# Performance work log

Hardware: AMD Instinct MI355X
Metric: run time of the kernel (lower is better)

The kernel has to match this reference:

```python
import jax, jax.numpy as jnp
import numpy as np

N_NODES = 50000
N_EDGES = 800000


def _gcn_norm(edge_index, n_nodes):
    # add self-loops, compute symmetric normalization D^-1/2 (A+I) D^-1/2
    loops = jnp.arange(n_nodes, dtype=edge_index.dtype)
    row = jnp.concatenate([edge_index[0], loops])
    col = jnp.concatenate([edge_index[1], loops])
    deg = jax.ops.segment_sum(jnp.ones_like(row, dtype=jnp.float32), row,
                              num_segments=n_nodes)
    dinv = jnp.where(deg > 0, jax.lax.rsqrt(deg), 0.0)
    norm = dinv[row] * dinv[col]  # [E+N]
    return row, col, norm


def _gcn_conv(x, W, b, row, col, norm, n_nodes):
    h = x @ W                                  # [N, out] transform first (cheaper gather)
    msg = norm[:, None] * h[col]               # [E+N, out]
    agg = jax.ops.segment_sum(msg, row, num_segments=n_nodes)
    return agg + b


def setup_inputs() -> dict:
    key = jax.random.key(0)
    ks = jax.random.split(key, 8)
    F_in, H, F_out = 64, 128, 64
    return {
        "features": jax.random.normal(ks[0], (N_NODES, F_in), jnp.float32),
        "W1": jax.random.normal(ks[1], (F_in, H), jnp.float32) / np.sqrt(F_in),
        "b1": jnp.zeros((H,), jnp.float32),
        "W2": jax.random.normal(ks[2], (H, H), jnp.float32) / np.sqrt(H),
        "b2": jnp.zeros((H,), jnp.float32),
        "W3": jax.random.normal(ks[3], (H, F_out), jnp.float32) / np.sqrt(H),
        "b3": jnp.zeros((F_out,), jnp.float32),
        "edge_index": jax.random.randint(ks[4], (2, N_EDGES), 0, N_NODES, jnp.int32),
    }


def reference(features, W1, b1, W2, b2, W3, b3, edge_index):
    n = features.shape[0]
    row, col, norm = _gcn_norm(edge_index, n)
    x = jax.nn.relu(_gcn_conv(features, W1, b1, row, col, norm, n))
    x = jax.nn.relu(_gcn_conv(x, W2, b2, row, col, norm, n))
    x = _gcn_conv(x, W3, b3, row, col, norm, n)
    return x
```

## Files before the change

### kernel.cpp

```cpp
#include <hip/hip_runtime.h>

#define N_NODES 50000
#define N_EDGES 800000

#define SCAN_CHUNK 256
#define SCAN_BLOCKS ((N_NODES + SCAN_CHUNK - 1) / SCAN_CHUNK)

static inline size_t alignUp(size_t x, size_t a) { return (x + a - 1) & ~(a - 1); }

typedef _Float16 h2 __attribute__((ext_vector_type(2)));
typedef _Float16 h4 __attribute__((ext_vector_type(4)));


__global__ void k_zero_i32(int* __restrict__ p, int n) {
    int i = blockIdx.x * 256 + threadIdx.x;
    if (i < n) p[i] = 0;
}

__global__ void k_count4(const int* __restrict__ row, int* __restrict__ count,
                         int* __restrict__ rank, int* __restrict__ pad) {
    int i = blockIdx.x * 256 + threadIdx.x;
    if (i < 64) pad[i] = 0;
    if (i < N_EDGES / 4) {
        int4 r = reinterpret_cast<const int4*>(row)[i];
        int k0 = atomicAdd(&count[r.x], 1);
        int k1 = atomicAdd(&count[r.y], 1);
        int k2 = atomicAdd(&count[r.z], 1);
        int k3 = atomicAdd(&count[r.w], 1);
        reinterpret_cast<int4*>(rank)[i] = make_int4(k0, k1, k2, k3);
    }
}

__global__ void k_blocksum(const int* __restrict__ count, int* __restrict__ bsum) {
    __shared__ int s[256];
    int t = threadIdx.x;
    int i = blockIdx.x * 256 + t;
    int v = (i < N_NODES) ? count[i] : 0;
    s[t] = v;
    __syncthreads();
    for (int off = 128; off > 0; off >>= 1) {
        if (t < off) s[t] += s[t + off];
        __syncthreads();
    }
    if (t == 0) bsum[blockIdx.x] = s[0];
}

__global__ void k_scan_bsum(int* __restrict__ bsum) {
    __shared__ int s[256];
    int t = threadIdx.x;
    int v = (t < SCAN_BLOCKS) ? bsum[t] : 0;
    s[t] = v;
    __syncthreads();
    for (int off = 1; off < 256; off <<= 1) {
        int add = (t >= off) ? s[t - off] : 0;
        __syncthreads();
        s[t] += add;
        __syncthreads();
    }
    if (t < SCAN_BLOCKS) bsum[t] = s[t] - v;
}

__global__ void k_scan_final(const int* __restrict__ count, const int* __restrict__ bsum,
                             int* __restrict__ offsets, float* __restrict__ dinv) {
    __shared__ int s[256];
    int t = threadIdx.x;
    int i = blockIdx.x * 256 + t;
    int v = (i < N_NODES) ? count[i] : 0;
    s[t] = v;
    __syncthreads();
    for (int off = 1; off < 256; off <<= 1) {
        int add = (t >= off) ? s[t - off] : 0;
        __syncthreads();
        s[t] += add;
        __syncthreads();
    }
    if (i < N_NODES) {
        offsets[i] = s[t] - v + bsum[blockIdx.x];
        dinv[i]    = rsqrtf((float)(v + 1));
    }
}

__global__ void k_scatter(const int* __restrict__ row, const int* __restrict__ col,
                          const int* __restrict__ offsets, const int* __restrict__ rank,
                          int* __restrict__ csr_col,
                          const float* __restrict__ feat, const float* __restrict__ dinv,
                          _Float16* __restrict__ featS) {
    int e = blockIdx.x * 256 + threadIdx.x;
    if (e < N_EDGES) {
        int node = e >> 4;
        float d = dinv[node];
        float4 v = reinterpret_cast<const float4*>(feat)[e];
        h4 hv = {(_Float16)(v.x * d), (_Float16)(v.y * d),
                 (_Float16)(v.z * d), (_Float16)(v.w * d)};
        reinterpret_cast<h4*>(featS)[e] = hv;
        int r = row[e];
        csr_col[offsets[r] + rank[e]] = col[e];
    }
}


template <bool BIAS>
__global__ __launch_bounds__(256) void k_agg128(const _Float16* __restrict__ hs, float* __restrict__ out,
        const int* __restrict__ csr_col, const int* __restrict__ offsets,
        const int* __restrict__ count, const float* __restrict__ dinv,
        const float* __restrict__ bias) {
    int lane = threadIdx.x & 63;
    int node = blockIdx.x * 4 + (threadIdx.x >> 6);
    const char* base = (const char*)hs;
    uint32_t lo = (uint32_t)lane << 2;

    float ax[8], ay[8];
#pragma unroll
    for (int u = 0; u < 8; u++) { ax[u] = 0.f; ay[u] = 0.f; }

    int n = count[node];
    const int* cp = csr_col + offsets[node];

    int e = 0;
    for (; e + 8 <= n; e += 8) {
        int c[8];
#pragma unroll
        for (int u = 0; u < 8; u++) c[u] = cp[e + u];
#pragma unroll
        for (int u = 0; u < 8; u++) {
            h2 v = *reinterpret_cast<const h2*>(base + (((uint32_t)c[u] << 8) + lo));
            ax[u] += (float)v.x; ay[u] += (float)v.y;
        }
    }
    if (e < n) {
        int c[8];
#pragma unroll
        for (int u = 0; u < 8; u++) c[u] = cp[e + u];
#pragma unroll
        for (int u = 0; u < 8; u++) {
            h2 v = *reinterpret_cast<const h2*>(base + (((uint32_t)c[u] << 8) + lo));
            if (e + u < n) { ax[u] += (float)v.x; ay[u] += (float)v.y; }
        }
    }

    float sx = 0.f, sy = 0.f;
#pragma unroll
    for (int u = 0; u < 8; u++) { sx += ax[u]; sy += ay[u]; }
    h2 self = *reinterpret_cast<const h2*>(base + (((uint32_t)node << 8) + lo));
    float d = dinv[node];
    float ox = (sx + (float)self.x) * d, oy = (sy + (float)self.y) * d;
    if (BIAS) { ox += bias[2 * lane]; oy += bias[2 * lane + 1]; }
    reinterpret_cast<float2*>(out)[(size_t)node * 64 + lane] = make_float2(ox, oy);
}

template <bool BIAS>
__global__ __launch_bounds__(256) void k_agg64(const _Float16* __restrict__ hs, float* __restrict__ out,
        const int* __restrict__ csr_col, const int* __restrict__ offsets,
        const int* __restrict__ count, const float* __restrict__ dinv,
        const float* __restrict__ bias) {
    int lane = threadIdx.x & 63;
    int node = blockIdx.x * 4 + (threadIdx.x >> 6);
    int q = lane >> 4;
    int f4 = lane & 15;
    const char* base = (const char*)hs;
    uint32_t fo = (uint32_t)f4 << 3;

    int n = __builtin_amdgcn_readfirstlane(count[node]);
    int start = __builtin_amdgcn_readfirstlane(offsets[node]);
    const int* cp = csr_col + start;

    float4 a0 = make_float4(0.f, 0.f, 0.f, 0.f);
    float4 a1 = make_float4(0.f, 0.f, 0.f, 0.f);

    int e = 0;
    for (; e + 32 <= n; e += 32) {
        int c[8];
#pragma unroll
        for (int u = 0; u < 8; u++) c[u] = cp[e + 4 * u + q];
        h4 v[8];
#pragma unroll
        for (int u = 0; u < 8; u++)
            v[u] = *reinterpret_cast<const h4*>(base + (((uint32_t)c[u] << 7) + fo));
#pragma unroll
        for (int u = 0; u < 8; u += 2) {
            a0.x += (float)v[u].x; a0.y += (float)v[u].y;
            a0.z += (float)v[u].z; a0.w += (float)v[u].w;
            a1.x += (float)v[u+1].x; a1.y += (float)v[u+1].y;
            a1.z += (float)v[u+1].z; a1.w += (float)v[u+1].w;
        }
    }
    if (e < n) {
        int c[8];
#pragma unroll
        for (int u = 0; u < 8; u++) c[u] = cp[e + 4 * u + q];
        h4 v[8];
#pragma unroll
        for (int u = 0; u < 8; u++)
            v[u] = *reinterpret_cast<const h4*>(base + (((uint32_t)c[u] << 7) + fo));
#pragma unroll
        for (int u = 0; u < 8; u++) {
            if (e + 4 * u + q < n) {
                a0.x += (float)v[u].x; a0.y += (float)v[u].y;
                a0.z += (float)v[u].z; a0.w += (float)v[u].w;
            }
        }
    }

    float sx = a0.x + a1.x, sy = a0.y + a1.y, sz = a0.z + a1.z, sw = a0.w + a1.w;
    sx += __shfl_xor(sx, 16); sy += __shfl_xor(sy, 16);
    sz += __shfl_xor(sz, 16); sw += __shfl_xor(sw, 16);
    sx += __shfl_xor(sx, 32); sy += __shfl_xor(sy, 32);
    sz += __shfl_xor(sz, 32); sw += __shfl_xor(sw, 32);
    if (q == 0) {
        h4 self = *reinterpret_cast<const h4*>(base + (((uint32_t)node << 7) + fo));
        float d = dinv[node];
        float ox = (sx + (float)self.x) * d, oy = (sy + (float)self.y) * d;
        float oz = (sz + (float)self.z) * d, ow = (sw + (float)self.w) * d;
        if (BIAS) {
            float4 bv = *reinterpret_cast<const float4*>(&bias[f4 * 4]);
            ox += bv.x; oy += bv.y; oz += bv.z; ow += bv.w;
        }
        *reinterpret_cast<float4*>((char*)out + ((uint32_t)node << 8) + (fo << 1)) =
            make_float4(ox, oy, oz, ow);
    }
}


template <int K, int NOUT, int BM, bool RELU, bool BIAS, bool SCALE, bool HOUT>
__global__ __launch_bounds__(256, 4) void k_gemm(const float* __restrict__ x,
        const float* __restrict__ W, const float* __restrict__ bias,
        const float* __restrict__ dinv, void* __restrict__ out, int nrows) {
    constexpr int BK = 32, BN = 64;
    constexpr int NCB = NOUT / BN;
    constexpr int RPT = BM / 16;
    __shared__ float xt[BK * BM];
    __shared__ float wt[BK * BN];

    int tid = threadIdx.x;
    int rg = tid & 15;
    int cg = tid >> 4;
    int row0 = (blockIdx.x / NCB) * BM;
    int col0 = (blockIdx.x % NCB) * BN;

    float acc[RPT][4] = {};

#pragma unroll 1
    for (int kk = 0; kk < K; kk += BK) {
        __syncthreads();
#pragma unroll
        for (int t = 0; t < BM / 32; ++t) {
            int idx = tid + t * 256;
            int r = idx >> 3;
            int kc = (idx & 7) * 4;
            float4 v = make_float4(0.f, 0.f, 0.f, 0.f);
            int gr = row0 + r;
            if (gr < nrows) v = *reinterpret_cast<const float4*>(&x[(size_t)gr * K + kk + kc]);
            int rc = r ^ kc;
            xt[(kc + 0) * BM + rc] = v.x;
            xt[(kc + 1) * BM + rc] = v.y;
            xt[(kc + 2) * BM + rc] = v.z;
            xt[(kc + 3) * BM + rc] = v.w;
        }
#pragma unroll
        for (int t = 0; t < 2; ++t) {
            int idx = tid + t * 256;
            int k = idx >> 4;
            int c = (idx & 15) * 4;
            *reinterpret_cast<float4*>(&wt[k * BN + c]) =
                *reinterpret_cast<const float4*>(&W[(size_t)(kk + k) * NOUT + col0 + c]);
        }
        __syncthreads();

#pragma unroll
        for (int k = 0; k < BK; ++k) {
            int s = k & 28;
            float4 wv = *reinterpret_cast<const float4*>(&wt[k * BN + cg * 4]);
            float wr[4] = {wv.x, wv.y, wv.z, wv.w};
            float xr[RPT];
            float4 x0 = *reinterpret_cast<const float4*>(&xt[k * BM + ((rg * 4) ^ s)]);
            xr[0] = x0.x; xr[1] = x0.y; xr[2] = x0.z; xr[3] = x0.w;
            if constexpr (RPT == 8) {
                float4 x1 = *reinterpret_cast<const float4*>(&xt[k * BM + (((rg * 4) ^ s) + 64)]);
                xr[4] = x1.x; xr[5] = x1.y; xr[6] = x1.z; xr[7] = x1.w;
            }
#pragma unroll
            for (int a = 0; a < RPT; a++)
#pragma unroll
                for (int b = 0; b < 4; b++) acc[a][b] += xr[a] * wr[b];
        }
    }

    float bv[4];
    if (BIAS) {
#pragma unroll
        for (int b = 0; b < 4; b++) bv[b] = bias[col0 + cg * 4 + b];
    }
#pragma unroll
    for (int a = 0; a < RPT; a++) {
        int r = rg * 4 + (a & 3) + ((a >= 4) ? 64 : 0);
        int gr = row0 + r;
        if (gr >= nrows) continue;
        float d = SCALE ? dinv[gr] : 1.f;
        float o[4];
#pragma unroll
        for (int b = 0; b < 4; b++) {
            float v = acc[a][b];
            if (BIAS) v += bv[b];
            if (RELU) v = fmaxf(v, 0.f);
            o[b] = v * d;
        }
        if constexpr (HOUT) {
            h4 ho = {(_Float16)o[0], (_Float16)o[1], (_Float16)o[2], (_Float16)o[3]};
            *reinterpret_cast<h4*>((_Float16*)out + (size_t)gr * NOUT + col0 + cg * 4) = ho;
        } else {
            *reinterpret_cast<float4*>((float*)out + (size_t)gr * NOUT + col0 + cg * 4) =
                make_float4(o[0], o[1], o[2], o[3]);
        }
    }
}


extern "C" void kernel_launch(void* const* d_in, const int* in_sizes, int n_in,
                              void* d_out, int out_size, void* d_ws, size_t ws_size,
                              hipStream_t stream) {
    const float* feat = (const float*)d_in[0];
    const float* W1 = (const float*)d_in[1];
    const float* b1 = (const float*)d_in[2];
    const float* W2 = (const float*)d_in[3];
    const float* b2 = (const float*)d_in[4];
    const float* W3 = (const float*)d_in[5];
    const float* b3 = (const float*)d_in[6];
    const int* ei = (const int*)d_in[7];
    const int* row = ei;
    const int* col = ei + N_EDGES;
    float* out = (float*)d_out;

    char* ws = (char*)d_ws;
    size_t off = 0;
    auto alloc = [&](size_t bytes) {
        void* p = ws + off;
        off = alignUp(off + bytes, 256);
        return p;
    };
    float* B0      = (float*)alloc((size_t)N_NODES * 128 * 4);
    float* B1      = (float*)alloc((size_t)N_NODES * 128 * 4);
    float* dinv    = (float*)alloc((size_t)N_NODES * 4);
    int*   count   = (int*)alloc((size_t)N_NODES * 4);
    int*   offsets = (int*)alloc((size_t)N_NODES * 4);
    int*   bsum    = (int*)alloc(1024);
    int*   csr_col = (int*)alloc((size_t)(N_EDGES + 64) * 4);
    int* rank = (int*)B0;
    _Float16* featS = (_Float16*)B1;
    _Float16* B1h = (_Float16*)B1;
    _Float16* B0h = (_Float16*)B0;

    const int eb = (N_EDGES + 255) / 256;
    const int cb4 = (N_EDGES / 4 + 255) / 256;
    const int rb128 = (N_NODES + 127) / 128;
    const int rb64  = (N_NODES + 63) / 64;
    const int agg_grid = N_NODES / 4;

    k_zero_i32<<<(N_NODES + 255) / 256, 256, 0, stream>>>(count, N_NODES);
    k_count4<<<cb4, 256, 0, stream>>>(row, count, rank, csr_col + N_EDGES);
    k_blocksum<<<SCAN_BLOCKS, 256, 0, stream>>>(count, bsum);
    k_scan_bsum<<<1, 256, 0, stream>>>(bsum);
    k_scan_final<<<SCAN_BLOCKS, 256, 0, stream>>>(count, bsum, offsets, dinv);
    k_scatter<<<eb, 256, 0, stream>>>(row, col, offsets, rank, csr_col, feat, dinv, featS);

    k_agg64<false><<<agg_grid, 256, 0, stream>>>(featS, B0, csr_col, offsets, count, dinv, nullptr);
    k_gemm<64, 128, 128, true, true, true, true><<<rb128 * 2, 256, 0, stream>>>(B0, W1, b1, dinv, B1h, N_NODES);

    k_agg128<false><<<agg_grid, 256, 0, stream>>>(B1h, B0, csr_col, offsets, count, dinv, nullptr);
    k_gemm<128, 128, 128, true, true, false, false><<<rb128 * 2, 256, 0, stream>>>(B0, W2, b2, dinv, B1, N_NODES);

    k_gemm<128, 64, 64, false, false, true, true><<<rb64, 256, 0, stream>>>(B1, W3, nullptr, dinv, B0h, N_NODES);
    k_agg64<true><<<agg_grid, 256, 0, stream>>>(B0h, out, csr_col, offsets, count, dinv, b3);
}
```

Before: 221.3 us.

## Replace FP32 SIMT GEMMs with FP16 MFMA GEMMs and store intermediates as FP16

The shared-memory FP32 tiled GEMM is replaced with a kernel that calls the 16x16x32 f16 MFMA instruction directly, reading A rows and pre-transposed FP16 weights straight from global memory. A new small kernel converts and transposes W1..W3 to FP16 on each call. The aggregation kernels gain an FP16 output mode, so every intermediate activation buffer is half precision, which halves the memory traffic between the aggregate and GEMM stages. In exchange, aggregated sums and the layer-2 output are rounded to FP16, which costs accuracy, and the GEMM gives up shared-memory reuse of the weight tile.

```diff
diff --git a/kernel.cpp b/kernel.cpp
--- a/kernel.cpp
+++ b/kernel.cpp
@@ -10,6 +10,8 @@
 
 typedef _Float16 h2 __attribute__((ext_vector_type(2)));
 typedef _Float16 h4 __attribute__((ext_vector_type(4)));
+typedef _Float16 h8 __attribute__((ext_vector_type(8)));
+typedef float    f4 __attribute__((ext_vector_type(4)));
 
 
 __global__ void k_zero_i32(int* __restrict__ p, int n) {
@@ -99,8 +101,25 @@
 }
 
 
-template <bool BIAS>
-__global__ __launch_bounds__(256) void k_agg128(const _Float16* __restrict__ hs, float* __restrict__ out,
+__global__ void k_prepw(const float* __restrict__ W1, const float* __restrict__ W2,
+                        const float* __restrict__ W3, _Float16* __restrict__ W1T,
+                        _Float16* __restrict__ W2T, _Float16* __restrict__ W3T) {
+    int i = blockIdx.x * 256 + threadIdx.x;
+    if (i < 8192) {
+        int n = i >> 6, k = i & 63;
+        W1T[i] = (_Float16)W1[k * 128 + n];
+    } else if (i < 24576) {
+        int j = i - 8192; int n = j >> 7, k = j & 127;
+        W2T[j] = (_Float16)W2[k * 128 + n];
+    } else {
+        int j = i - 24576; int n = j >> 7, k = j & 127;
+        W3T[j] = (_Float16)W3[k * 64 + n];
+    }
+}
+
+
+template <bool BIAS, bool HOUT>
+__global__ __launch_bounds__(256) void k_agg128(const _Float16* __restrict__ hs, void* __restrict__ out,
         const int* __restrict__ csr_col, const int* __restrict__ offsets,
         const int* __restrict__ count, const float* __restrict__ dinv,
         const float* __restrict__ bias) {
@@ -145,11 +164,16 @@
     float d = dinv[node];
     float ox = (sx + (float)self.x) * d, oy = (sy + (float)self.y) * d;
     if (BIAS) { ox += bias[2 * lane]; oy += bias[2 * lane + 1]; }
-    reinterpret_cast<float2*>(out)[(size_t)node * 64 + lane] = make_float2(ox, oy);
-}
-
-template <bool BIAS>
-__global__ __launch_bounds__(256) void k_agg64(const _Float16* __restrict__ hs, float* __restrict__ out,
+    if constexpr (HOUT) {
+        h2 hv = {(_Float16)ox, (_Float16)oy};
+        reinterpret_cast<h2*>(out)[(size_t)node * 64 + lane] = hv;
+    } else {
+        reinterpret_cast<float2*>(out)[(size_t)node * 64 + lane] = make_float2(ox, oy);
+    }
+}
+
+template <bool BIAS, bool HOUT>
+__global__ __launch_bounds__(256) void k_agg64(const _Float16* __restrict__ hs, void* __restrict__ out,
         const int* __restrict__ csr_col, const int* __restrict__ offsets,
         const int* __restrict__ count, const float* __restrict__ dinv,
         const float* __restrict__ bias) {
@@ -215,101 +239,64 @@
             float4 bv = *reinterpret_cast<const float4*>(&bias[f4 * 4]);
             ox += bv.x; oy += bv.y; oz += bv.z; ow += bv.w;
         }
-        *reinterpret_cast<float4*>((char*)out + ((uint32_t)node << 8) + (fo << 1)) =
-            make_float4(ox, oy, oz, ow);
-    }
-}
-
-
-template <int K, int NOUT, int BM, bool RELU, bool BIAS, bool SCALE, bool HOUT>
-__global__ __launch_bounds__(256, 4) void k_gemm(const float* __restrict__ x,
-        const float* __restrict__ W, const float* __restrict__ bias,
+        if constexpr (HOUT) {
+            h4 hv = {(_Float16)ox, (_Float16)oy, (_Float16)oz, (_Float16)ow};
+            *reinterpret_cast<h4*>((char*)out + (((uint32_t)node << 7) + fo)) = hv;
+        } else {
+            *reinterpret_cast<float4*>((char*)out + ((uint32_t)node << 8) + (fo << 1)) =
+                make_float4(ox, oy, oz, ow);
+        }
+    }
+}
+
+
+template <int K, int NOUT, bool RELU, bool BIAS, bool SCALE, bool HOUT>
+__global__ __launch_bounds__(256) void k_gemm_mfma(const _Float16* __restrict__ x,
+        const _Float16* __restrict__ WT, const float* __restrict__ bias,
         const float* __restrict__ dinv, void* __restrict__ out, int nrows) {
-    constexpr int BK = 32, BN = 64;
-    constexpr int NCB = NOUT / BN;
-    constexpr int RPT = BM / 16;
-    __shared__ float xt[BK * BM];
-    __shared__ float wt[BK * BN];
-
-    int tid = threadIdx.x;
-    int rg = tid & 15;
-    int cg = tid >> 4;
-    int row0 = (blockIdx.x / NCB) * BM;
-    int col0 = (blockIdx.x % NCB) * BN;
-
-    float acc[RPT][4] = {};
-
-#pragma unroll 1
-    for (int kk = 0; kk < K; kk += BK) {
-        __syncthreads();
-#pragma unroll
-        for (int t = 0; t < BM / 32; ++t) {
-            int idx = tid + t * 256;
-            int r = idx >> 3;
-            int kc = (idx & 7) * 4;
-            float4 v = make_float4(0.f, 0.f, 0.f, 0.f);
-            int gr = row0 + r;
-            if (gr < nrows) v = *reinterpret_cast<const float4*>(&x[(size_t)gr * K + kk + kc]);
-            int rc = r ^ kc;
-            xt[(kc + 0) * BM + rc] = v.x;
-            xt[(kc + 1) * BM + rc] = v.y;
-            xt[(kc + 2) * BM + rc] = v.z;
-            xt[(kc + 3) * BM + rc] = v.w;
-        }
-#pragma unroll
-        for (int t = 0; t < 2; ++t) {
-            int idx = tid + t * 256;
-            int k = idx >> 4;
-            int c = (idx & 15) * 4;
-            *reinterpret_cast<float4*>(&wt[k * BN + c]) =
-                *reinterpret_cast<const float4*>(&W[(size_t)(kk + k) * NOUT + col0 + c]);
-        }
-        __syncthreads();
-
-#pragma unroll
-        for (int k = 0; k < BK; ++k) {
-            int s = k & 28;
-            float4 wv = *reinterpret_cast<const float4*>(&wt[k * BN + cg * 4]);
-            float wr[4] = {wv.x, wv.y, wv.z, wv.w};
-            float xr[RPT];
-            float4 x0 = *reinterpret_cast<const float4*>(&xt[k * BM + ((rg * 4) ^ s)]);
-            xr[0] = x0.x; xr[1] = x0.y; xr[2] = x0.z; xr[3] = x0.w;
-            if constexpr (RPT == 8) {
-                float4 x1 = *reinterpret_cast<const float4*>(&xt[k * BM + (((rg * 4) ^ s) + 64)]);
-                xr[4] = x1.x; xr[5] = x1.y; xr[6] = x1.z; xr[7] = x1.w;
-            }
-#pragma unroll
-            for (int a = 0; a < RPT; a++)
-#pragma unroll
-                for (int b = 0; b < 4; b++) acc[a][b] += xr[a] * wr[b];
-        }
-    }
-
-    float bv[4];
-    if (BIAS) {
-#pragma unroll
-        for (int b = 0; b < 4; b++) bv[b] = bias[col0 + cg * 4 + b];
-    }
-#pragma unroll
-    for (int a = 0; a < RPT; a++) {
-        int r = rg * 4 + (a & 3) + ((a >= 4) ? 64 : 0);
-        int gr = row0 + r;
-        if (gr >= nrows) continue;
-        float d = SCALE ? dinv[gr] : 1.f;
-        float o[4];
-#pragma unroll
-        for (int b = 0; b < 4; b++) {
-            float v = acc[a][b];
-            if (BIAS) v += bv[b];
+    constexpr int NB = NOUT / 16;
+    int l = threadIdx.x & 63;
+    int w = threadIdx.x >> 6;
+    int lm = l & 15;
+    int kb = (l >> 4) * 8;
+    int row0 = blockIdx.x * 64 + w * 16;
+
+    int arow = row0 + lm;
+    if (arow >= nrows) arow = nrows - 1;
+
+    f4 acc[NB] = {};
+
+#pragma unroll
+    for (int kk = 0; kk < K / 32; ++kk) {
+        h8 a = *reinterpret_cast<const h8*>(x + (size_t)arow * K + kk * 32 + kb);
+#pragma unroll
+        for (int n = 0; n < NB; ++n) {
+            h8 b = *reinterpret_cast<const h8*>(WT + (size_t)(n * 16 + lm) * K + kk * 32 + kb);
+            acc[n] = __builtin_amdgcn_mfma_f32_16x16x32_f16(a, b, acc[n], 0, 0, 0);
+        }
+    }
+
+    int rbase = row0 + (l >> 4) * 4;
+    float dv[4];
+#pragma unroll
+    for (int t = 0; t < 4; ++t) {
+        int gr = rbase + t;
+        dv[t] = SCALE ? dinv[(gr < nrows) ? gr : (nrows - 1)] : 1.f;
+    }
+#pragma unroll
+    for (int n = 0; n < NB; ++n) {
+        float bvn = BIAS ? bias[n * 16 + lm] : 0.f;
+#pragma unroll
+        for (int t = 0; t < 4; ++t) {
+            int gr = rbase + t;
+            if (gr >= nrows) continue;
+            float v = acc[n][t] + bvn;
             if (RELU) v = fmaxf(v, 0.f);
-            o[b] = v * d;
-        }
-        if constexpr (HOUT) {
-            h4 ho = {(_Float16)o[0], (_Float16)o[1], (_Float16)o[2], (_Float16)o[3]};
-            *reinterpret_cast<h4*>((_Float16*)out + (size_t)gr * NOUT + col0 + cg * 4) = ho;
-        } else {
-            *reinterpret_cast<float4*>((float*)out + (size_t)gr * NOUT + col0 + cg * 4) =
-                make_float4(o[0], o[1], o[2], o[3]);
+            v *= dv[t];
+            if constexpr (HOUT)
+                ((_Float16*)out)[(size_t)gr * NOUT + n * 16 + lm] = (_Float16)v;
+            else
+                ((float*)out)[(size_t)gr * NOUT + n * 16 + lm] = v;
         }
     }
 }
@@ -337,23 +324,33 @@
         off = alignUp(off + bytes, 256);
         return p;
     };
-    float* B0      = (float*)alloc((size_t)N_NODES * 128 * 4);
-    float* B1      = (float*)alloc((size_t)N_NODES * 128 * 4);
+    constexpr size_t SLOT = (size_t)N_NODES * 128 * 2;
+    _Float16* S1 = (_Float16*)alloc(SLOT);
+    _Float16* S2 = (_Float16*)alloc(SLOT);
+    _Float16* S3 = (_Float16*)alloc(SLOT);
     float* dinv    = (float*)alloc((size_t)N_NODES * 4);
     int*   count   = (int*)alloc((size_t)N_NODES * 4);
     int*   offsets = (int*)alloc((size_t)N_NODES * 4);
     int*   bsum    = (int*)alloc(1024);
+    int*   rank    = (int*)alloc((size_t)N_EDGES * 4);
     int*   csr_col = (int*)alloc((size_t)(N_EDGES + 64) * 4);
-    int* rank = (int*)B0;
-    _Float16* featS = (_Float16*)B1;
-    _Float16* B1h = (_Float16*)B1;
-    _Float16* B0h = (_Float16*)B0;
+    _Float16* W1T  = (_Float16*)alloc(128 * 64 * 2);
+    _Float16* W2T  = (_Float16*)alloc(128 * 128 * 2);
+    _Float16* W3T  = (_Float16*)alloc(64 * 128 * 2);
+
+    _Float16* featS = S1;
+    _Float16* A1h = S2;
+    _Float16* X1h = S1;
+    _Float16* A2h = S2;
+    _Float16* X2h = S3;
+    _Float16* H3h = S1;
 
     const int eb = (N_EDGES + 255) / 256;
     const int cb4 = (N_EDGES / 4 + 255) / 256;
-    const int rb128 = (N_NODES + 127) / 128;
-    const int rb64  = (N_NODES + 63) / 64;
+    const int gemm_grid = (N_NODES + 63) / 64;
     const int agg_grid = N_NODES / 4;
+
+    k_prepw<<<128, 256, 0, stream>>>(W1, W2, W3, W1T, W2T, W3T);
 
     k_zero_i32<<<(N_NODES + 255) / 256, 256, 0, stream>>>(count, N_NODES);
     k_count4<<<cb4, 256, 0, stream>>>(row, count, rank, csr_col + N_EDGES);
@@ -362,12 +359,12 @@
     k_scan_final<<<SCAN_BLOCKS, 256, 0, stream>>>(count, bsum, offsets, dinv);
     k_scatter<<<eb, 256, 0, stream>>>(row, col, offsets, rank, csr_col, feat, dinv, featS);
 
-    k_agg64<false><<<agg_grid, 256, 0, stream>>>(featS, B0, csr_col, offsets, count, dinv, nullptr);
-    k_gemm<64, 128, 128, true, true, true, true><<<rb128 * 2, 256, 0, stream>>>(B0, W1, b1, dinv, B1h, N_NODES);
-
-    k_agg128<false><<<agg_grid, 256, 0, stream>>>(B1h, B0, csr_col, offsets, count, dinv, nullptr);
-    k_gemm<128, 128, 128, true, true, false, false><<<rb128 * 2, 256, 0, stream>>>(B0, W2, b2, dinv, B1, N_NODES);
-
-    k_gemm<128, 64, 64, false, false, true, true><<<rb64, 256, 0, stream>>>(B1, W3, nullptr, dinv, B0h, N_NODES);
-    k_agg64<true><<<agg_grid, 256, 0, stream>>>(B0h, out, csr_col, offsets, count, dinv, b3);
-}
+    k_agg64<false, true><<<agg_grid, 256, 0, stream>>>(featS, A1h, csr_col, offsets, count, dinv, nullptr);
+    k_gemm_mfma<64, 128, true, true, true, true><<<gemm_grid, 256, 0, stream>>>(A1h, W1T, b1, dinv, X1h, N_NODES);
+
+    k_agg128<false, true><<<agg_grid, 256, 0, stream>>>(X1h, A2h, csr_col, offsets, count, dinv, nullptr);
+    k_gemm_mfma<128, 128, true, true, false, true><<<gemm_grid, 256, 0, stream>>>(A2h, W2T, b2, dinv, X2h, N_NODES);
+
+    k_gemm_mfma<128, 64, false, false, true, true><<<gemm_grid, 256, 0, stream>>>(X2h, W3T, nullptr, dinv, H3h, N_NODES);
+    k_agg64<true, false><<<agg_grid, 256, 0, stream>>>(H3h, out, csr_col, offsets, count, dinv, b3);
+}
```

New measurement: 208.9 us (median of 2 runs). 5.6% less time.
